# Kernel tuning notes

Hardware: AMD Instinct MI355X
Metric: run time of the kernel (lower is better)

Reference implementation:

```python
import jax, jax.numpy as jnp
import numpy as np

B, T, E = 4, 2048, 512
H, D = 8, 64            # num_heads, head_size = E // H
HID = H * E             # FFN hidden = num_heads * n_embed (per source)
EPS = 1e-5


def layer_norm(x, g, b):
    mu = jnp.mean(x, axis=-1, keepdims=True)
    var = jnp.var(x, axis=-1, keepdims=True)
    return (x - mu) * jax.lax.rsqrt(var + EPS) * g + b


def setup_inputs() -> dict:
    key = jax.random.key(0)
    ks = jax.random.split(key, 12)
    s_e = 1.0 / np.sqrt(E)
    s_hd = 1.0 / np.sqrt(H * D)
    s_hid = 1.0 / np.sqrt(HID)
    return {
        "x": jax.random.normal(ks[0], (B, T, E), jnp.float32),
        "Wq": jax.random.normal(ks[1], (H, E, D), jnp.float32) * s_e,
        "Wk": jax.random.normal(ks[2], (H, E, D), jnp.float32) * s_e,
        "Wv": jax.random.normal(ks[3], (H, E, D), jnp.float32) * s_e,
        "Wo": jax.random.normal(ks[4], (H * D, E), jnp.float32) * s_hd,
        "bo": jnp.zeros((E,), jnp.float32),
        "W1": jax.random.normal(ks[5], (E, HID), jnp.float32) * s_e,
        "b1": jnp.zeros((HID,), jnp.float32),
        "W2": jax.random.normal(ks[6], (HID, E), jnp.float32) * s_hid,
        "b2": jnp.zeros((E,), jnp.float32),
        "g1": jnp.ones((E,), jnp.float32),
        "be1": jnp.zeros((E,), jnp.float32),
        "g2": jnp.ones((E,), jnp.float32),
        "be2": jnp.zeros((E,), jnp.float32),
    }


def reference(x, Wq, Wk, Wv, Wo, bo, W1, b1, W2, b2, g1, be1, g2, be2):
    # pre-LN decoder block (layer_norm_first=True path)
    xn = layer_norm(x, g1, be1)

    # multi-head causal attention; NOTE: scale is T**-0.5 per the source code
    q = jnp.einsum('bte,hed->bhtd', xn, Wq)
    k = jnp.einsum('bte,hed->bhtd', xn, Wk)
    v = jnp.einsum('bte,hed->bhtd', xn, Wv)
    scores = jnp.einsum('bhtd,bhsd->bhts', q, k) * (T ** -0.5)
    causal = jnp.tril(jnp.ones((T, T), bool))
    scores = jnp.where(causal, scores, -jnp.inf)
    attn = jax.nn.softmax(scores, axis=-1)
    o = jnp.einsum('bhts,bhsd->bhtd', attn, v)           # [B,H,T,D]
    o = o.transpose(0, 2, 1, 3).reshape(B, T, H * D)      # concat heads
    mha = o @ Wo + bo

    x = xn + mha
    xn2 = layer_norm(x, g2, be2)
    ffn = jax.nn.relu(xn2 @ W1 + b1) @ W2 + b2
    return xn2 + ffn
```

## Files before the change

kernel.cpp:

```cpp
#include <hip/hip_runtime.h>
#include <hip/hip_bf16.h>
#include <math.h>

#define Bsz 4
#define Tt 2048
#define Ee 512
#define Hh 8
#define Dd 64
#define HIDs 4096
#define Mrows (Bsz * Tt)

typedef __attribute__((ext_vector_type(8))) short short8;
typedef __attribute__((ext_vector_type(4))) float f32x4;
typedef __attribute__((ext_vector_type(16))) float f32x16;

#define AS1 __attribute__((address_space(1)))
#define AS3 __attribute__((address_space(3)))

__device__ __forceinline__ unsigned short f2bfu(float f) {
    unsigned u = __float_as_uint(f);
    return (unsigned short)((u + 0x7fffu + ((u >> 16) & 1u)) >> 16);
}
__device__ __forceinline__ unsigned short truncbf(float f) {
    return (unsigned short)(__float_as_uint(f) >> 16);
}

__device__ __forceinline__ short8 ld_sw(const __hip_bfloat16* base, int R, int sl) {
    return *(const short8*)(base + R * 32 + (((sl) ^ ((R >> 1) & 3)) << 3));
}

__device__ __forceinline__ void ln_body(const float* __restrict__ x,
        const float* __restrict__ g, const float* __restrict__ b,
        const float* __restrict__ addb,
        float* __restrict__ out_f, __hip_bfloat16* __restrict__ out_bf,
        int row) {
    int tid = threadIdx.x;
    const float* xr = x + (size_t)row * Ee;
    float v0 = xr[tid];
    float v1 = xr[tid + 256];
    float s = v0 + v1;
    float sq = v0 * v0 + v1 * v1;
#pragma unroll
    for (int off = 32; off > 0; off >>= 1) {
        s  += __shfl_xor(s, off, 64);
        sq += __shfl_xor(sq, off, 64);
    }
    __shared__ float ls[4], lq[4];
    int wid = tid >> 6, lane = tid & 63;
    if (lane == 0) { ls[wid] = s; lq[wid] = sq; }
    __syncthreads();
    s  = ls[0] + ls[1] + ls[2] + ls[3];
    sq = lq[0] + lq[1] + lq[2] + lq[3];
    float mean = s * (1.0f / Ee);
    float var  = sq * (1.0f / Ee) - mean * mean;
    float rstd = rsqrtf(var + 1e-5f);
    float o0 = (v0 - mean) * rstd * g[tid]       + b[tid];
    float o1 = (v1 - mean) * rstd * g[tid + 256] + b[tid + 256];
    float* orow = out_f + (size_t)row * Ee;
    orow[tid]       = o0 + addb[tid];
    orow[tid + 256] = o1 + addb[tid + 256];
    __hip_bfloat16* brow = out_bf + (size_t)row * Ee;
    brow[tid]       = __float2bfloat16(o0);
    brow[tid + 256] = __float2bfloat16(o1);
}

__global__ __launch_bounds__(256) void ln_kernel(const float* __restrict__ x,
        const float* __restrict__ g, const float* __restrict__ b,
        const float* __restrict__ addb,
        float* __restrict__ out_f, __hip_bfloat16* __restrict__ out_bf) {
    ln_body(x, g, b, addb, out_f, out_bf, blockIdx.x);
}

__device__ __forceinline__ void tr_tile(const float* __restrict__ in,
        __hip_bfloat16* __restrict__ outp, int R, int C, int c0, int r0) {
    __shared__ float tile[64][65];
    int tc = threadIdx.x & 63, tg = threadIdx.x >> 6;
#pragma unroll
    for (int i = 0; i < 16; ++i) {
        int r = tg * 16 + i;
        tile[r][tc] = in[(size_t)(r0 + r) * C + c0 + tc];
    }
    __syncthreads();
#pragma unroll
    for (int i = 0; i < 16; ++i) {
        int cc = tg * 16 + i;
        outp[(size_t)(c0 + cc) * R + r0 + tc] = __float2bfloat16(tile[tc][cc]);
    }
}
__global__ __launch_bounds__(256) void startup_kernel(
        const float* __restrict__ x, const float* __restrict__ g1,
        const float* __restrict__ be1, const float* __restrict__ bo,
        float* __restrict__ xn, __hip_bfloat16* __restrict__ xn_bf,
        const float* __restrict__ Wq, const float* __restrict__ Wk,
        const float* __restrict__ Wv, const float* __restrict__ Wo,
        const float* __restrict__ W1, const float* __restrict__ W2,
        __hip_bfloat16* __restrict__ bqT, __hip_bfloat16* __restrict__ woT,
        __hip_bfloat16* __restrict__ w1T, __hip_bfloat16* __restrict__ w2T) {
    if (blockIdx.x < Mrows) {
        ln_body(x, g1, be1, bo, xn, xn_bf, blockIdx.x);
        return;
    }
    int blk = blockIdx.x - Mrows;
    if (blk < 192) {
        int p = blk >> 6, h = (blk >> 3) & 7, et = blk & 7;
        const float* W = (p == 0) ? Wq : ((p == 1) ? Wk : Wv);
        float sc = (p == 0) ? 0.022097086912079608f * 1.4426950408889634f : 1.0f;
        __shared__ float tile[64][65];
        int td = threadIdx.x & 63, tg = threadIdx.x >> 6;
#pragma unroll
        for (int i = 0; i < 16; ++i) {
            int e = tg * 16 + i;
            tile[e][td] = W[((size_t)h * Ee + et * 64 + e) * Dd + td] * sc;
        }
        __syncthreads();
#pragma unroll
        for (int i = 0; i < 16; ++i) {
            int d = tg * 16 + i;
            bqT[((size_t)(p * 512 + h * 64 + d)) * Ee + et * 64 + td] =
                __float2bfloat16(tile[td][d]);
        }
    } else if (blk < 256) {
        int t = blk - 192;
        tr_tile(Wo, woT, 512, 512, (t & 7) * 64, (t >> 3) * 64);
    } else if (blk < 768) {
        int t = blk - 256;
        tr_tile(W1, w1T, 512, HIDs, (t & 63) * 64, (t >> 6) * 64);
    } else {
        int t = blk - 768;
        tr_tile(W2, w2T, HIDs, 512, (t & 7) * 64, (t >> 3) * 64);
    }
}

__global__ __launch_bounds__(256) void mfma_gemm(
        const __hip_bfloat16* __restrict__ A, int lda,
        const __hip_bfloat16* __restrict__ B, int ldb,
        __hip_bfloat16* __restrict__ Cb, int ldc, int K, int nx) {
    __shared__ __hip_bfloat16 S[32768];
    int tid = threadIdx.x;
    int lane = tid & 63, wave = tid >> 6;
    int wm = wave >> 1, wn = wave & 1;
    int L = blockIdx.x;
    int slots = (int)gridDim.x >> 3;
    int v = (L & 7) * slots + (L >> 3);
    int bx = v % nx, by = v / nx;
    int row0 = by * 128, col0 = bx * 128;
    f32x4 acc[4][4];
#pragma unroll
    for (int i = 0; i < 4; ++i)
#pragma unroll
        for (int j = 0; j < 4; ++j) acc[i][j] = (f32x4){0.f, 0.f, 0.f, 0.f};

    int fr = lane & 15, sl = lane >> 4;
    int T = K >> 6;

#define STAGEQ(tt, bb)                                                        \
    do {                                                                      \
        int kk_ = (tt) * 64;                                                  \
        _Pragma("unroll")                                                     \
        for (int j = 0; j < 4; ++j) {                                         \
            int c = j * 256 + tid;                                            \
            int p = c >> 9, cp = c & 511;                                     \
            int r = cp >> 2, s = cp & 3;                                      \
            int kg = ((s ^ ((r >> 1) & 3)) << 3);                             \
            int cb = j * 256 + wave * 64;                                     \
            int ko = kk_ + p * 32 + kg;                                       \
            __builtin_amdgcn_global_load_lds(                                 \
                (const AS1 void*)(A + (size_t)(row0 + r) * lda + ko),         \
                (AS3 void*)(S + (bb) * 16384 + cb * 8), 16, 0, 0);            \
            __builtin_amdgcn_global_load_lds(                                 \
                (const AS1 void*)(B + (size_t)(col0 + r) * ldb + ko),         \
                (AS3 void*)(S + (bb) * 16384 + 8192 + cb * 8), 16, 0, 0);     \
        }                                                                     \
    } while (0)

    STAGEQ(0, 0);
    for (int t = 0; t < T; ++t) {
        int tn = (t + 1 < T) ? t + 1 : 0;
        STAGEQ(tn, (t + 1) & 1);
        asm volatile("s_waitcnt vmcnt(8)" ::: "memory");
        __builtin_amdgcn_s_barrier();
        asm volatile("" ::: "memory");
        const __hip_bfloat16* Ab = S + (t & 1) * 16384;
        const __hip_bfloat16* Bb = Ab + 8192;
#pragma unroll
        for (int ks = 0; ks < 2; ++ks) {
            short8 afr[4], bfr[4];
#pragma unroll
            for (int i = 0; i < 4; ++i) {
                afr[i] = ld_sw(Ab + ks * 4096, wm * 64 + i * 16 + fr, sl);
                bfr[i] = ld_sw(Bb + ks * 4096, wn * 64 + i * 16 + fr, sl);
            }
#pragma unroll
            for (int i = 0; i < 4; ++i)
#pragma unroll
                for (int j = 0; j < 4; ++j)
                    acc[i][j] = __builtin_amdgcn_mfma_f32_16x16x32_bf16(afr[i], bfr[j], acc[i][j], 0, 0, 0);
        }
        asm volatile("" ::: "memory");
        __builtin_amdgcn_s_barrier();
        asm volatile("" ::: "memory");
    }
#undef STAGEQ
    asm volatile("s_waitcnt vmcnt(0)" ::: "memory");
    __syncthreads();
    unsigned short* Ew = (unsigned short*)S + wave * 1152;
    const __hip_bfloat16* Er = (const __hip_bfloat16*)Ew;
    int rq = (lane >> 4) << 2;
    int rr = lane >> 2, cb2 = (lane & 3) * 16;
#pragma unroll
    for (int i = 0; i < 4; ++i) {
#pragma unroll
        for (int j = 0; j < 4; ++j)
#pragma unroll
            for (int gi = 0; gi < 4; ++gi)
                Ew[(rq + gi) * 72 + j * 16 + fr] = f2bfu(acc[i][j][gi]);
        uint4 v0 = *(const uint4*)(Er + rr * 72 + cb2);
        uint4 v1 = *(const uint4*)(Er + rr * 72 + cb2 + 8);
        size_t rg = (size_t)(row0 + wm * 64 + i * 16 + rr) * ldc + col0 + wn * 64 + cb2;
        *(uint4*)(Cb + rg)     = v0;
        *(uint4*)(Cb + rg + 8) = v1;
    }
}

__global__ __launch_bounds__(256) void mfma_gemm_n64(
        const __hip_bfloat16* __restrict__ A, int lda,
        const __hip_bfloat16* __restrict__ B, int ldb,
        float* __restrict__ Cf, int ldc, int K, int nx) {
    __shared__ __hip_bfloat16 S[36864];
    int tid = threadIdx.x;
    int lane = tid & 63, wave = tid >> 6;
    int L = blockIdx.x;
    int slots = (int)gridDim.x >> 3;
    int v = (L & 7) * slots + (L >> 3);
    int bx = v % nx, by = v / nx;
    int row0 = by * 128, col0 = bx * 64;
    f32x4 acc[2][4];
#pragma unroll
    for (int i = 0; i < 2; ++i)
#pragma unroll
        for (int j = 0; j < 4; ++j) acc[i][j] = (f32x4){0.f, 0.f, 0.f, 0.f};

    int fr = lane & 15, sl = lane >> 4;
    int T = K >> 6;

#define STAGEN(tt, bb)                                                        \
    do {                                                                      \
        int kk_ = (tt) * 64;                                                  \
        _Pragma("unroll")                                                     \
        for (int j = 0; j < 4; ++j) {                                         \
            int c = j * 256 + tid;                                            \
            int p = c >> 9, cp = c & 511;                                     \
            int r = cp >> 2, s = cp & 3;                                      \
            int kg = ((s ^ ((r >> 1) & 3)) << 3);                             \
            int cb = j * 256 + wave * 64;                                     \
            __builtin_amdgcn_global_load_lds(                                 \
                (const AS1 void*)(A + (size_t)(row0 + r) * lda + kk_ + p * 32 + kg), \
                (AS3 void*)(S + (bb) * 12288 + cb * 8), 16, 0, 0);            \
        }                                                                     \
        _Pragma("unroll")                                                     \
        for (int j = 0; j < 2; ++j) {                                         \
            int c = j * 256 + tid;                                            \
            int p = c >> 8, cp = c & 255;                                     \
            int r = cp >> 2, s = cp & 3;                                      \
            int kg = ((s ^ ((r >> 1) & 3)) << 3);                             \
            int cb = j * 256 + wave * 64;                                     \
            __builtin_amdgcn_global_load_lds(                                 \
                (const AS1 void*)(B + (size_t)(col0 + r) * ldb + kk_ + p * 32 + kg), \
                (AS3 void*)(S + (bb) * 12288 + 8192 + cb * 8), 16, 0, 0);     \
        }                                                                     \
    } while (0)

    STAGEN(0, 0);
    STAGEN(1, 1);
    for (int t = 0; t < T; ++t) {
        int tn = (t + 2 < T) ? t + 2 : 0;
        STAGEN(tn, (t + 2) % 3);
        asm volatile("s_waitcnt vmcnt(12)" ::: "memory");
        __builtin_amdgcn_s_barrier();
        asm volatile("" ::: "memory");
        const __hip_bfloat16* Ab = S + (t % 3) * 12288;
        const __hip_bfloat16* Bb = Ab + 8192;
#pragma unroll
        for (int ks = 0; ks < 2; ++ks) {
            short8 afr[2], bfr[4];
#pragma unroll
            for (int i = 0; i < 2; ++i)
                afr[i] = ld_sw(Ab + ks * 4096, wave * 32 + i * 16 + fr, sl);
#pragma unroll
            for (int j = 0; j < 4; ++j)
                bfr[j] = ld_sw(Bb + ks * 2048, j * 16 + fr, sl);
#pragma unroll
            for (int i = 0; i < 2; ++i)
#pragma unroll
                for (int j = 0; j < 4; ++j)
                    acc[i][j] = __builtin_amdgcn_mfma_f32_16x16x32_bf16(afr[i], bfr[j], acc[i][j], 0, 0, 0);
        }
        asm volatile("" ::: "memory");
        __builtin_amdgcn_s_barrier();
        asm volatile("" ::: "memory");
    }
#undef STAGEN
    asm volatile("s_waitcnt vmcnt(0)" ::: "memory");
    int rq = (lane >> 4) << 2;
#pragma unroll
    for (int i = 0; i < 2; ++i)
#pragma unroll
        for (int j = 0; j < 4; ++j)
#pragma unroll
            for (int gidx = 0; gidx < 4; ++gidx) {
                int r = row0 + wave * 32 + i * 16 + rq + gidx;
                int c = col0 + j * 16 + fr;
                Cf[(size_t)r * ldc + c] += acc[i][j][gidx];
            }
}

__global__ __launch_bounds__(256, 1) void gemm_n256(
        const __hip_bfloat16* __restrict__ A, int lda,
        const __hip_bfloat16* __restrict__ B, int ldb,
        float* __restrict__ Cf, int ldc, int Ksp) {
    __shared__ __hip_bfloat16 S[3 * 24576];
    int tid = threadIdx.x;
    int lane = tid & 63, wave = tid >> 6;
    int wm = wave >> 1, wn = wave & 1;
    int L = blockIdx.x;
    int slots = (int)gridDim.x >> 3;
    int v = (L & 7) * slots + (L >> 3);
    int kq = v & 1;
    int u = v >> 1;
    int bx = u & 1, by = u >> 1;
    int row0 = by * 128, col0 = bx * 256;
    A += (size_t)kq * Ksp;
    B += (size_t)kq * Ksp;
    f32x4 acc[4][8];
#pragma unroll
    for (int i = 0; i < 4; ++i)
#pragma unroll
        for (int j = 0; j < 8; ++j) acc[i][j] = (f32x4){0.f, 0.f, 0.f, 0.f};

    int fr = lane & 15, sl = lane >> 4;
    int T = Ksp >> 6;

#define STG256(tt, bb)                                                        \
    do {                                                                      \
        int kk_ = (tt) * 64;                                                  \
        _Pragma("unroll")                                                     \
        for (int j = 0; j < 4; ++j) {                                         \
            int c = j * 256 + tid;                                            \
            int p = c >> 9, cp = c & 511;                                     \
            int r = cp >> 2, s = cp & 3;                                      \
            int kg = ((s ^ ((r >> 1) & 3)) << 3);                             \
            int cb = j * 256 + wave * 64;                                     \
            __builtin_amdgcn_global_load_lds(                                 \
                (const AS1 void*)(A + (size_t)(row0 + r) * lda + kk_ + p * 32 + kg), \
                (AS3 void*)(S + (bb) * 24576 + cb * 8), 16, 0, 0);            \
        }                                                                     \
        _Pragma("unroll")                                                     \
        for (int j = 0; j < 8; ++j) {                                         \
            int c = j * 256 + tid;                                            \
            int p = c >> 10, cp = c & 1023;                                   \
            int r = cp >> 2, s = cp & 3;                                      \
            int kg = ((s ^ ((r >> 1) & 3)) << 3);                             \
            int cb = j * 256 + wave * 64;                                     \
            __builtin_amdgcn_global_load_lds(                                 \
                (const AS1 void*)(B + (size_t)(col0 + r) * ldb + kk_ + p * 32 + kg), \
                (AS3 void*)(S + (bb) * 24576 + 8192 + cb * 8), 16, 0, 0);     \
        }                                                                     \
    } while (0)

    STG256(0, 0);
    STG256(1, 1);
    for (int t = 0; t < T; ++t) {
        int tn = (t + 2 < T) ? t + 2 : 0;
        STG256(tn, (t + 2) % 3);
        asm volatile("s_waitcnt vmcnt(24)" ::: "memory");
        __builtin_amdgcn_s_barrier();
        asm volatile("" ::: "memory");
        const __hip_bfloat16* Ab = S + (t % 3) * 24576;
        const __hip_bfloat16* Bb = Ab + 8192;
#pragma unroll
        for (int ks = 0; ks < 2; ++ks) {
            short8 afr[4], bfr[8];
#pragma unroll
            for (int i = 0; i < 4; ++i)
                afr[i] = ld_sw(Ab + ks * 4096, wm * 64 + i * 16 + fr, sl);
#pragma unroll
            for (int j = 0; j < 8; ++j)
                bfr[j] = ld_sw(Bb + ks * 8192, wn * 128 + j * 16 + fr, sl);
#pragma unroll
            for (int i = 0; i < 4; ++i)
#pragma unroll
                for (int j = 0; j < 8; ++j)
                    acc[i][j] = __builtin_amdgcn_mfma_f32_16x16x32_bf16(afr[i], bfr[j], acc[i][j], 0, 0, 0);
        }
        asm volatile("" ::: "memory");
        __builtin_amdgcn_s_barrier();
        asm volatile("" ::: "memory");
    }
#undef STG256
    asm volatile("s_waitcnt vmcnt(0)" ::: "memory");
    int rq = (lane >> 4) << 2;
#pragma unroll
    for (int i = 0; i < 4; ++i)
#pragma unroll
        for (int j = 0; j < 8; ++j)
#pragma unroll
            for (int gi = 0; gi < 4; ++gi) {
                int r = row0 + wm * 64 + i * 16 + rq + gi;
                int c = col0 + wn * 128 + j * 16 + fr;
                unsafeAtomicAdd(&Cf[(size_t)r * ldc + c], acc[i][j][gi]);
            }
}

__device__ __forceinline__ short8 ld_frag(const __hip_bfloat16* base, int r, int slot) {
    return *(const short8*)(base + r * 64 + ((slot ^ (r & 7)) << 3));
}

__global__ __launch_bounds__(512, 2) void gemm256_8ph(
        const __hip_bfloat16* __restrict__ A, int lda,
        const __hip_bfloat16* __restrict__ B, int ldb,
        __hip_bfloat16* __restrict__ Cb, int ldc, int K,
        const float* __restrict__ bias, int nx) {
    __shared__ __hip_bfloat16 S[65536];
    __hip_bfloat16* Asb = S;
    __hip_bfloat16* Bsb = S + 32768;
    int tid = threadIdx.x;
    int lane = tid & 63, wave = tid >> 6;
    int wm = wave >> 2, wn = wave & 3;
    int fr = lane & 15, l5 = lane >> 4;
    int L = blockIdx.x;
    int slots = (int)gridDim.x >> 3;
    int v = (L & 7) * slots + (L >> 3);
    int bx = v % nx, by = v / nx;
    int row0 = by * 256, col0 = bx * 256;
    int T = K >> 6;

    f32x4 acc[8][4];
#pragma unroll
    for (int i = 0; i < 8; ++i)
#pragma unroll
        for (int j = 0; j < 4; ++j) acc[i][j] = (f32x4){0.f, 0.f, 0.f, 0.f};

#define STAGE_A(tt, hh, bb)                                                   \
    do {                                                                      \
        _Pragma("unroll")                                                     \
        for (int j = 0; j < 2; ++j) {                                         \
            int c = j * 512 + tid;                                            \
            int r = c >> 3;                                                   \
            int sl = (c & 7) ^ (r & 7);                                       \
            int cb = j * 512 + wave * 64;                                     \
            int grow = row0 + ((r >> 6) << 7) + (hh) * 64 + (r & 63);         \
            __builtin_amdgcn_global_load_lds(                                 \
                (const AS1 void*)(A + (size_t)grow * lda + (tt) * 64 + sl * 8), \
                (AS3 void*)(Asb + (bb) * 16384 + (hh) * 8192 + cb * 8), 16, 0, 0); \
        }                                                                     \
    } while (0)
#define STAGE_B(tt, hh, bb)                                                   \
    do {                                                                      \
        _Pragma("unroll")                                                     \
        for (int j = 0; j < 2; ++j) {                                         \
            int c = j * 512 + tid;                                            \
            int r = c >> 3;                                                   \
            int sl = (c & 7) ^ (r & 7);                                       \
            int cb = j * 512 + wave * 64;                                     \
            int gcol = col0 + ((r >> 5) << 6) + (hh) * 32 + (r & 31);         \
            __builtin_amdgcn_global_load_lds(                                 \
                (const AS1 void*)(B + (size_t)gcol * ldb + (tt) * 64 + sl * 8), \
                (AS3 void*)(Bsb + (bb) * 16384 + (hh) * 8192 + cb * 8), 16, 0, 0); \
        }                                                                     \
    } while (0)

    STAGE_A(0, 0, 0);
    STAGE_B(0, 0, 0);
    STAGE_B(0, 1, 0);
    STAGE_A(0, 1, 0);

    short8 a[4][2], b[2][2][2];
    for (int t = 0; t < T; ++t) {
        int buf = t & 1, nb = buf ^ 1;
        int tn = (t + 1 < T) ? t + 1 : 0;
        const __hip_bfloat16* Ab0 = Asb + buf * 16384;
        const __hip_bfloat16* Ab1 = Ab0 + 8192;
        const __hip_bfloat16* Bb0 = Bsb + buf * 16384;
        const __hip_bfloat16* Bb1 = Bb0 + 8192;

        STAGE_A(tn, 0, nb);
        asm volatile("s_waitcnt vmcnt(6)" ::: "memory");
        __builtin_amdgcn_s_barrier();
        asm volatile("" ::: "memory");
#pragma unroll
        for (int i = 0; i < 4; ++i)
#pragma unroll
            for (int ks = 0; ks < 2; ++ks)
                a[i][ks] = ld_frag(Ab0, wm * 64 + i * 16 + fr, ks * 4 + l5);
#pragma unroll
        for (int jj = 0; jj < 2; ++jj)
#pragma unroll
            for (int ks = 0; ks < 2; ++ks)
                b[0][jj][ks] = ld_frag(Bb0, wn * 32 + jj * 16 + fr, ks * 4 + l5);
        __builtin_amdgcn_s_setprio(1);
#pragma unroll
        for (int i = 0; i < 4; ++i)
#pragma unroll
            for (int jj = 0; jj < 2; ++jj)
#pragma unroll
                for (int ks = 0; ks < 2; ++ks)
                    acc[i][jj] = __builtin_amdgcn_mfma_f32_16x16x32_bf16(
                        a[i][ks], b[0][jj][ks], acc[i][jj], 0, 0, 0);
        __builtin_amdgcn_s_setprio(0);
        asm volatile("" ::: "memory");
        __builtin_amdgcn_s_barrier();
        asm volatile("" ::: "memory");

        STAGE_B(tn, 0, nb);
        asm volatile("s_waitcnt vmcnt(6)" ::: "memory");
        __builtin_amdgcn_s_barrier();
        asm volatile("" ::: "memory");
#pragma unroll
        for (int jj = 0; jj < 2; ++jj)
#pragma unroll
            for (int ks = 0; ks < 2; ++ks)
                b[1][jj][ks] = ld_frag(Bb1, wn * 32 + jj * 16 + fr, ks * 4 + l5);
        __builtin_amdgcn_s_setprio(1);
#pragma unroll
        for (int i = 0; i < 4; ++i)
#pragma unroll
            for (int jj = 0; jj < 2; ++jj)
#pragma unroll
                for (int ks = 0; ks < 2; ++ks)
                    acc[i][2 + jj] = __builtin_amdgcn_mfma_f32_16x16x32_bf16(
                        a[i][ks], b[1][jj][ks], acc[i][2 + jj], 0, 0, 0);
        __builtin_amdgcn_s_setprio(0);
        asm volatile("" ::: "memory");
        __builtin_amdgcn_s_barrier();
        asm volatile("" ::: "memory");

        STAGE_B(tn, 1, nb);
        asm volatile("s_waitcnt vmcnt(6)" ::: "memory");
        __builtin_amdgcn_s_barrier();
        asm volatile("" ::: "memory");
#pragma unroll
        for (int i = 0; i < 4; ++i)
#pragma unroll
            for (int ks = 0; ks < 2; ++ks)
                a[i][ks] = ld_frag(Ab1, wm * 64 + i * 16 + fr, ks * 4 + l5);
        __builtin_amdgcn_s_setprio(1);
#pragma unroll
        for (int i = 0; i < 4; ++i)
#pragma unroll
            for (int jj = 0; jj < 2; ++jj)
#pragma unroll
                for (int ks = 0; ks < 2; ++ks)
                    acc[4 + i][2 + jj] = __builtin_amdgcn_mfma_f32_16x16x32_bf16(
                        a[i][ks], b[1][jj][ks], acc[4 + i][2 + jj], 0, 0, 0);
        __builtin_amdgcn_s_setprio(0);
        asm volatile("" ::: "memory");
        __builtin_amdgcn_s_barrier();
        asm volatile("" ::: "memory");

        STAGE_A(tn, 1, nb);
        asm volatile("" ::: "memory");
        __builtin_amdgcn_s_barrier();
        asm volatile("" ::: "memory");
        __builtin_amdgcn_s_setprio(1);
#pragma unroll
        for (int i = 0; i < 4; ++i)
#pragma unroll
            for (int jj = 0; jj < 2; ++jj)
#pragma unroll
                for (int ks = 0; ks < 2; ++ks)
                    acc[4 + i][jj] = __builtin_amdgcn_mfma_f32_16x16x32_bf16(
                        a[i][ks], b[0][jj][ks], acc[4 + i][jj], 0, 0, 0);
        __builtin_amdgcn_s_setprio(0);
        asm volatile("" ::: "memory");
        __builtin_amdgcn_s_barrier();
        asm volatile("" ::: "memory");
    }
#undef STAGE_A
#undef STAGE_B

    __syncthreads();
    float bvv[4];
#pragma unroll
    for (int nj = 0; nj < 4; ++nj) bvv[nj] = bias[col0 + wn * 64 + nj * 16 + fr];
    unsigned short* Ew = (unsigned short*)S + wave * 1152;
    const __hip_bfloat16* Er = (const __hip_bfloat16*)Ew;
    int rq = l5 << 2;
    int rr = lane >> 2, cb2 = (lane & 3) * 16;
#pragma unroll
    for (int mi = 0; mi < 8; ++mi) {
#pragma unroll
        for (int nj = 0; nj < 4; ++nj)
#pragma unroll
            for (int gi = 0; gi < 4; ++gi) {
                float tv = acc[mi][nj][gi] + bvv[nj];
                Ew[(rq + gi) * 72 + nj * 16 + fr] = f2bfu(tv > 0.f ? tv : 0.f);
            }
        uint4 v0 = *(const uint4*)(Er + rr * 72 + cb2);
        uint4 v1 = *(const uint4*)(Er + rr * 72 + cb2 + 8);
        size_t rg = (size_t)(row0 + wm * 128 + mi * 16 + rr) * ldc
                    + col0 + wn * 64 + cb2;
        *(uint4*)(Cb + rg)     = v0;
        *(uint4*)(Cb + rg + 8) = v1;
    }
}

__global__ __launch_bounds__(256) void attn_mfma(const __hip_bfloat16* __restrict__ qkvb,
        __hip_bfloat16* __restrict__ ob) {
    __shared__ __hip_bfloat16 KsS[2][64 * 72];
    __shared__ __hip_bfloat16 VtS[2][64 * 72];
    __shared__ __hip_bfloat16 PsS[4 * 32 * 72];
    __hip_bfloat16* Qs = PsS;

    const unsigned short* q16 = (const unsigned short*)qkvb;
    int tid  = threadIdx.x;
    int lane = tid & 63, wave = tid >> 6;
    int l31 = lane & 31, l5 = lane >> 5;
    int blk = blockIdx.x;
    int qb  = 15 - (blk >> 5);
    int bh  = blk & 31;
    int b = bh >> 3, h = bh & 7;
    int base = qb * 128;
    size_t tokbase = (size_t)b * Tt;
    int qoff = h * 64, koff = 512 + h * 64, voff = 1024 + h * 64;

    {
        int q = tid >> 1, dg = (tid & 1) * 32;
        const unsigned short* src = q16 + (tokbase + base + q) * 1536 + qoff + dg;
        uint4 a  = *(const uint4*)src;
        uint4 b4 = *(const uint4*)(src + 8);
        uint4 c4 = *(const uint4*)(src + 16);
        uint4 d4 = *(const uint4*)(src + 24);
        *(uint4*)(Qs + q * 72 + dg)      = a;
        *(uint4*)(Qs + q * 72 + dg + 8)  = b4;
        *(uint4*)(Qs + q * 72 + dg + 16) = c4;
        *(uint4*)(Qs + q * 72 + dg + 24) = d4;
    }
    __syncthreads();
    short8 aq[4];
#pragma unroll
    for (int kd = 0; kd < 4; ++kd)
        aq[kd] = *(const short8*)(Qs + (wave * 32 + l31) * 72 + kd * 16 + l5 * 8);

    short8 ones;
#pragma unroll
    for (int i = 0; i < 8; ++i) ones[i] = (short)0x3F80;

    f32x16 acc[2], accL;
#pragma unroll
    for (int i = 0; i < 16; ++i) { acc[0][i] = 0.f; acc[1][i] = 0.f; accL[i] = 0.f; }
    __hip_bfloat16* Psw = PsS + wave * (32 * 72);
    unsigned short* Psw16 = (unsigned short*)Psw;

    int s_k = tid >> 2, dg_k = (tid & 3) * 16;
    int sp = (tid & 31) * 2, dg8 = (tid >> 5) * 8;
    uint4 kr0, kr1, va, vb;
    {
        const unsigned short* kp = q16 + (tokbase + s_k) * 1536 + koff + dg_k;
        kr0 = *(const uint4*)kp;
        kr1 = *(const uint4*)(kp + 8);
        const unsigned short* vp = q16 + (tokbase + sp) * 1536 + voff + dg8;
        va = *(const uint4*)vp;
        vb = *(const uint4*)(vp + 1536);
    }

    int tmax = 2 * qb + 1;
    for (int tile = 0; tile <= tmax; ++tile) {
        int buf = tile & 1;
        *(uint4*)(KsS[buf] + s_k * 72 + dg_k)     = kr0;
        *(uint4*)(KsS[buf] + s_k * 72 + dg_k + 8) = kr1;
        {
            unsigned a0[4] = {va.x, va.y, va.z, va.w};
            unsigned b0[4] = {vb.x, vb.y, vb.z, vb.w};
#pragma unroll
            for (int i = 0; i < 4; ++i) {
                unsigned p0 = (a0[i] & 0xffffu) | (b0[i] << 16);
                unsigned p1 = (a0[i] >> 16) | (b0[i] & 0xffff0000u);
                *(unsigned*)(VtS[buf] + (dg8 + 2 * i) * 72 + sp)     = p0;
                *(unsigned*)(VtS[buf] + (dg8 + 2 * i + 1) * 72 + sp) = p1;
            }
        }
        __syncthreads();
        if (tile < tmax) {
            int s1 = (tile + 1) * 64;
            const unsigned short* kp = q16 + (tokbase + s1 + s_k) * 1536 + koff + dg_k;
            kr0 = *(const uint4*)kp;
            kr1 = *(const uint4*)(kp + 8);
            const unsigned short* vp = q16 + (tokbase + s1 + sp) * 1536 + voff + dg8;
            va = *(const uint4*)vp;
            vb = *(const uint4*)(vp + 1536);
        }
        if (tile == tmax && wave < 2) continue;
        f32x16 Sc[2];
#pragma unroll
        for (int i = 0; i < 16; ++i) { Sc[0][i] = 0.f; Sc[1][i] = 0.f; }
#pragma unroll
        for (int st = 0; st < 2; ++st)
#pragma unroll
            for (int kd = 0; kd < 4; ++kd) {
                short8 bk = *(const short8*)(KsS[buf] + (st * 32 + l31) * 72 + kd * 16 + l5 * 8);
                Sc[st] = __builtin_amdgcn_mfma_f32_32x32x16_bf16(aq[kd], bk, Sc[st], 0, 0, 0);
            }
        if (tile >= 2 * qb) {
            int s0t = tile * 64;
            int qrb = base + wave * 32 + 4 * l5;
#pragma unroll
            for (int st = 0; st < 2; ++st) {
                int sg = s0t + st * 32 + l31;
#pragma unroll
                for (int reg = 0; reg < 16; ++reg) {
                    int qr = qrb + (reg & 3) + 8 * (reg >> 2);
                    if (sg > qr) Sc[st][reg] = -1e30f;
                }
            }
        }
#pragma unroll
        for (int st = 0; st < 2; ++st)
#pragma unroll
            for (int reg = 0; reg < 16; ++reg) {
                int pr = (reg & 3) + 8 * (reg >> 2) + 4 * l5;
                Psw16[pr * 72 + st * 32 + l31] =
                    truncbf(__builtin_amdgcn_exp2f(Sc[st][reg]));
            }
#pragma unroll
        for (int ks = 0; ks < 4; ++ks) {
            short8 ap = *(const short8*)(Psw + l31 * 72 + ks * 16 + l5 * 8);
            accL = __builtin_amdgcn_mfma_f32_32x32x16_bf16(ap, ones, accL, 0, 0, 0);
#pragma unroll
            for (int dt = 0; dt < 2; ++dt) {
                short8 bv = *(const short8*)(VtS[buf] + (dt * 32 + l31) * 72 + ks * 16 + l5 * 8);
                acc[dt] = __builtin_amdgcn_mfma_f32_32x32x16_bf16(ap, bv, acc[dt], 0, 0, 0);
            }
        }
    }
#pragma unroll
    for (int reg = 0; reg < 16; ++reg) {
        float rl = 1.0f / accL[reg];
        int qr = base + wave * 32 + (reg & 3) + 8 * (reg >> 2) + 4 * l5;
#pragma unroll
        for (int dt = 0; dt < 2; ++dt)
            ob[(tokbase + qr) * 512 + h * 64 + dt * 32 + l31] =
                __float2bfloat16(acc[dt][reg] * rl);
    }
}

extern "C" void kernel_launch(void* const* d_in, const int* in_sizes, int n_in,
                              void* d_out, int out_size, void* d_ws, size_t ws_size,
                              hipStream_t stream) {
    const float* x   = (const float*)d_in[0];
    const float* Wq  = (const float*)d_in[1];
    const float* Wk  = (const float*)d_in[2];
    const float* Wv  = (const float*)d_in[3];
    const float* Wo  = (const float*)d_in[4];
    const float* bo  = (const float*)d_in[5];
    const float* W1  = (const float*)d_in[6];
    const float* b1  = (const float*)d_in[7];
    const float* W2  = (const float*)d_in[8];
    const float* b2  = (const float*)d_in[9];
    const float* g1  = (const float*)d_in[10];
    const float* be1 = (const float*)d_in[11];
    const float* g2  = (const float*)d_in[12];
    const float* be2 = (const float*)d_in[13];
    float* out = (float*)d_out;

    char* ws = (char*)d_ws;
    __hip_bfloat16* bqT    = (__hip_bfloat16*)(ws);
    __hip_bfloat16* woT    = (__hip_bfloat16*)(ws + 1572864);
    __hip_bfloat16* w1T    = (__hip_bfloat16*)(ws + 2097152);
    __hip_bfloat16* w2T    = (__hip_bfloat16*)(ws + 6291456);
    float*          xn     = (float*)(ws + 10485760);
    __hip_bfloat16* xn_bf  = (__hip_bfloat16*)(ws + 27262976);
    __hip_bfloat16* qkv_bf = (__hip_bfloat16*)(ws + 35651584);
    __hip_bfloat16* o_bf   = (__hip_bfloat16*)(ws + 60817408);
    __hip_bfloat16* h_bf   = (__hip_bfloat16*)(ws + 35651584);

    startup_kernel<<<Mrows + 1280, 256, 0, stream>>>(
        x, g1, be1, bo, xn, xn_bf, Wq, Wk, Wv, Wo, W1, W2, bqT, woT, w1T, w2T);
    mfma_gemm<<<768, 256, 0, stream>>>(
        xn_bf, 512, bqT, 512, qkv_bf, 1536, 512, 12);
    attn_mfma<<<Bsz * Hh * (Tt / 128), 256, 0, stream>>>(qkv_bf, o_bf);
    mfma_gemm_n64<<<512, 256, 0, stream>>>(
        o_bf, 512, woT, 512, xn, 512, 512, 8);
    ln_kernel<<<Mrows, 256, 0, stream>>>(xn, g2, be2, b2, out, xn_bf);
    gemm256_8ph<<<512, 512, 0, stream>>>(
        xn_bf, 512, w1T, 512, h_bf, HIDs, 512, b1, 16);
    gemm_n256<<<256, 256, 0, stream>>>(
        h_bf, HIDs, w2T, HIDs, out, 512, 2048);
}
```

Measured before the change: 325.9 us.

## Replace split-K 128x256 FFN2 GEMM with 64x128 full-K tiles and plain stores

```diff
diff --git a/kernel.cpp b/kernel.cpp
--- a/kernel.cpp
+++ b/kernel.cpp
@@ -314,35 +314,42 @@
             }
 }
 
-__global__ __launch_bounds__(256, 1) void gemm_n256(
+__global__ __launch_bounds__(256) void gemm_m64n128(
         const __hip_bfloat16* __restrict__ A, int lda,
         const __hip_bfloat16* __restrict__ B, int ldb,
-        float* __restrict__ Cf, int ldc, int Ksp) {
-    __shared__ __hip_bfloat16 S[3 * 24576];
+        float* __restrict__ Cf, int ldc, int K, int nx) {
+    __shared__ __hip_bfloat16 S[36864];
     int tid = threadIdx.x;
     int lane = tid & 63, wave = tid >> 6;
     int wm = wave >> 1, wn = wave & 1;
     int L = blockIdx.x;
     int slots = (int)gridDim.x >> 3;
     int v = (L & 7) * slots + (L >> 3);
-    int kq = v & 1;
-    int u = v >> 1;
-    int bx = u & 1, by = u >> 1;
-    int row0 = by * 128, col0 = bx * 256;
-    A += (size_t)kq * Ksp;
-    B += (size_t)kq * Ksp;
-    f32x4 acc[4][8];
-#pragma unroll
-    for (int i = 0; i < 4; ++i)
-#pragma unroll
-        for (int j = 0; j < 8; ++j) acc[i][j] = (f32x4){0.f, 0.f, 0.f, 0.f};
+    int bx = v % nx, by = v / nx;
+    int row0 = by * 64, col0 = bx * 128;
+    f32x4 acc[2][4];
+#pragma unroll
+    for (int i = 0; i < 2; ++i)
+#pragma unroll
+        for (int j = 0; j < 4; ++j) acc[i][j] = (f32x4){0.f, 0.f, 0.f, 0.f};
 
     int fr = lane & 15, sl = lane >> 4;
-    int T = Ksp >> 6;
-
-#define STG256(tt, bb)                                                        \
+    int T = K >> 6;
+
+#define STAGEW(tt, bb)                                                        \
     do {                                                                      \
         int kk_ = (tt) * 64;                                                  \
+        _Pragma("unroll")                                                     \
+        for (int j = 0; j < 2; ++j) {                                         \
+            int c = j * 256 + tid;                                            \
+            int p = c >> 8, cp = c & 255;                                     \
+            int r = cp >> 2, s = cp & 3;                                      \
+            int kg = ((s ^ ((r >> 1) & 3)) << 3);                             \
+            int cb = j * 256 + wave * 64;                                     \
+            __builtin_amdgcn_global_load_lds(                                 \
+                (const AS1 void*)(A + (size_t)(row0 + r) * lda + kk_ + p * 32 + kg), \
+                (AS3 void*)(S + (bb) * 12288 + cb * 8), 16, 0, 0);            \
+        }                                                                     \
         _Pragma("unroll")                                                     \
         for (int j = 0; j < 4; ++j) {                                         \
             int c = j * 256 + tid;                                            \
@@ -351,63 +358,52 @@
             int kg = ((s ^ ((r >> 1) & 3)) << 3);                             \
             int cb = j * 256 + wave * 64;                                     \
             __builtin_amdgcn_global_load_lds(                                 \
-                (const AS1 void*)(A + (size_t)(row0 + r) * lda + kk_ + p * 32 + kg), \
-                (AS3 void*)(S + (bb) * 24576 + cb * 8), 16, 0, 0);            \
-        }                                                                     \
-        _Pragma("unroll")                                                     \
-        for (int j = 0; j < 8; ++j) {                                         \
-            int c = j * 256 + tid;                                            \
-            int p = c >> 10, cp = c & 1023;                                   \
-            int r = cp >> 2, s = cp & 3;                                      \
-            int kg = ((s ^ ((r >> 1) & 3)) << 3);                             \
-            int cb = j * 256 + wave * 64;                                     \
-            __builtin_amdgcn_global_load_lds(                                 \
                 (const AS1 void*)(B + (size_t)(col0 + r) * ldb + kk_ + p * 32 + kg), \
-                (AS3 void*)(S + (bb) * 24576 + 8192 + cb * 8), 16, 0, 0);     \
+                (AS3 void*)(S + (bb) * 12288 + 4096 + cb * 8), 16, 0, 0);     \
         }                                                                     \
     } while (0)
 
-    STG256(0, 0);
-    STG256(1, 1);
+    STAGEW(0, 0);
+    STAGEW(1, 1);
     for (int t = 0; t < T; ++t) {
         int tn = (t + 2 < T) ? t + 2 : 0;
-        STG256(tn, (t + 2) % 3);
-        asm volatile("s_waitcnt vmcnt(24)" ::: "memory");
-        __builtin_amdgcn_s_barrier();
-        asm volatile("" ::: "memory");
-        const __hip_bfloat16* Ab = S + (t % 3) * 24576;
-        const __hip_bfloat16* Bb = Ab + 8192;
+        STAGEW(tn, (t + 2) % 3);
+        asm volatile("s_waitcnt vmcnt(12)" ::: "memory");
+        __builtin_amdgcn_s_barrier();
+        asm volatile("" ::: "memory");
+        const __hip_bfloat16* Ab = S + (t % 3) * 12288;
+        const __hip_bfloat16* Bb = Ab + 4096;
 #pragma unroll
         for (int ks = 0; ks < 2; ++ks) {
-            short8 afr[4], bfr[8];
-#pragma unroll
-            for (int i = 0; i < 4; ++i)
-                afr[i] = ld_sw(Ab + ks * 4096, wm * 64 + i * 16 + fr, sl);
-#pragma unroll
-            for (int j = 0; j < 8; ++j)
-                bfr[j] = ld_sw(Bb + ks * 8192, wn * 128 + j * 16 + fr, sl);
-#pragma unroll
-            for (int i = 0; i < 4; ++i)
-#pragma unroll
-                for (int j = 0; j < 8; ++j)
+            short8 afr[2], bfr[4];
+#pragma unroll
+            for (int i = 0; i < 2; ++i)
+                afr[i] = ld_sw(Ab + ks * 2048, wm * 32 + i * 16 + fr, sl);
+#pragma unroll
+            for (int j = 0; j < 4; ++j)
+                bfr[j] = ld_sw(Bb + ks * 4096, wn * 64 + j * 16 + fr, sl);
+#pragma unroll
+            for (int i = 0; i < 2; ++i)
+#pragma unroll
+                for (int j = 0; j < 4; ++j)
                     acc[i][j] = __builtin_amdgcn_mfma_f32_16x16x32_bf16(afr[i], bfr[j], acc[i][j], 0, 0, 0);
         }
         asm volatile("" ::: "memory");
         __builtin_amdgcn_s_barrier();
         asm volatile("" ::: "memory");
     }
-#undef STG256
+#undef STAGEW
     asm volatile("s_waitcnt vmcnt(0)" ::: "memory");
     int rq = (lane >> 4) << 2;
 #pragma unroll
-    for (int i = 0; i < 4; ++i)
-#pragma unroll
-        for (int j = 0; j < 8; ++j)
-#pragma unroll
-            for (int gi = 0; gi < 4; ++gi) {
-                int r = row0 + wm * 64 + i * 16 + rq + gi;
-                int c = col0 + wn * 128 + j * 16 + fr;
-                unsafeAtomicAdd(&Cf[(size_t)r * ldc + c], acc[i][j][gi]);
+    for (int i = 0; i < 2; ++i)
+#pragma unroll
+        for (int j = 0; j < 4; ++j)
+#pragma unroll
+            for (int gidx = 0; gidx < 4; ++gidx) {
+                int r = row0 + wm * 32 + i * 16 + rq + gidx;
+                int c = col0 + wn * 64 + j * 16 + fr;
+                Cf[(size_t)r * ldc + c] += acc[i][j][gidx];
             }
 }
 
@@ -783,6 +779,6 @@
     ln_kernel<<<Mrows, 256, 0, stream>>>(xn, g2, be2, b2, out, xn_bf);
     gemm256_8ph<<<512, 512, 0, stream>>>(
         xn_bf, 512, w1T, 512, h_bf, HIDs, 512, b1, 16);
-    gemm_n256<<<256, 256, 0, stream>>>(
-        h_bf, HIDs, w2T, HIDs, out, 512, 2048);
-}
+    gemm_m64n128<<<512, 256, 0, stream>>>(
+        h_bf, HIDs, w2T, HIDs, out, 512, HIDs, 4);
+}
```

Result: faster. 295.9 us (-9.2%).
